# Kernel optimization log

Hardware: AMD Instinct MI355X
Metric: run time of the kernel (lower is better)

## Reference

```python
import jax, jax.numpy as jnp
import numpy as np

N_PTS = 1_000_000
N_CORNERS = 2_000_000  # per-level corner count (table has +1 zero row for misses)
FEAT_DIM = 16
MAX_LEVEL = 12
FEAT_LEVELS = 3  # levels MAX_LEVEL, MAX_LEVEL-1, MAX_LEVEL-2
POLY_INT = True


def setup_inputs() -> dict:
    key = jax.random.key(0)
    ks = jax.random.split(key, 8)
    x = jax.random.uniform(ks[0], (N_PTS, 3), jnp.float32, -1.0, 1.0)
    std = 0.05
    feats = [std * jax.random.normal(ks[1 + i], (N_CORNERS + 1, FEAT_DIM), jnp.float32)
             for i in range(FEAT_LEVELS)]
    # last row is the zero feature for unobserved nodes
    feats = [f.at[-1].set(0.0) for f in feats]
    idxs = [jax.random.randint(ks[4 + i], (N_PTS, 8), 0, N_CORNERS, dtype=jnp.int64)
            for i in range(FEAT_LEVELS)]
    return {"x": x,
            "feat0": feats[0], "feat1": feats[1], "feat2": feats[2],
            "idx0": idxs[0], "idx1": idxs[1], "idx2": idxs[2]}


def _interp_coeffs(x, level, polynomial_on=POLY_INT):
    # coords = 2^level * (x*0.5 + 0.5); d = frac(coords)
    coords = (2.0 ** level) * (x * 0.5 + 0.5)
    d = coords - jnp.floor(coords)                      # [N,3]
    t = 3.0 * d**2 - 2.0 * d**3 if polynomial_on else d
    tx, ty, tz = t[:, 0], t[:, 1], t[:, 2]
    ux, uy, uz = 1.0 - tx, 1.0 - ty, 1.0 - tz
    # corner order matches torch.stack((p0..p7)): z fastest, then y, then x
    p = jnp.stack([ux * uy * uz, ux * uy * tz, ux * ty * uz, ux * ty * tz,
                   tx * uy * uz, tx * uy * tz, tx * ty * uz, tx * ty * tz],
                  axis=1)                               # [N,8]
    return p


def reference(x, feat0, feat1, feat2, idx0, idx1, idx2):
    feats = (feat0, feat1, feat2)
    idxs = (idx0, idx1, idx2)
    out = jnp.zeros((x.shape[0], FEAT_DIM), dtype=x.dtype)
    for i in range(FEAT_LEVELS):
        level = MAX_LEVEL - i
        p = _interp_coeffs(x, level)                    # [N,8]
        g = feats[i][idxs[i]]                           # [N,8,D] gather
        out = out + jnp.einsum("nk,nkd->nd", p, g)
    return out
```

## Files before the change

### kernel.cpp

```cpp
#include <hip/hip_runtime.h>


__device__ __forceinline__ void accum_level(
    long long pt, int sub, float cx, float cy, float cz,
    const float4* __restrict__ feat, const int* __restrict__ idx,
    float4& acc)
{
    float dx = cx - floorf(cx);
    float dy = cy - floorf(cy);
    float dz = cz - floorf(cz);
    float tx = dx * dx * (3.0f - 2.0f * dx);
    float ty = dy * dy * (3.0f - 2.0f * dy);
    float tz = dz * dz * (3.0f - 2.0f * dz);
    float ux = 1.0f - tx, uy = 1.0f - ty, uz = 1.0f - tz;

    float p[8];
    p[0] = ux * uy * uz;
    p[1] = ux * uy * tz;
    p[2] = ux * ty * uz;
    p[3] = ux * ty * tz;
    p[4] = tx * uy * uz;
    p[5] = tx * uy * tz;
    p[6] = tx * ty * uz;
    p[7] = tx * ty * tz;

    const int4* iv = (const int4*)(idx + pt * 8);
    int4 ia = iv[0];
    int4 ib = iv[1];
    int id[8] = { ia.x, ia.y, ia.z, ia.w, ib.x, ib.y, ib.z, ib.w };

#pragma unroll
    for (int k = 0; k < 8; ++k) {
        float4 g = feat[(long long)id[k] * 4 + sub];
        acc.x = fmaf(p[k], g.x, acc.x);
        acc.y = fmaf(p[k], g.y, acc.y);
        acc.z = fmaf(p[k], g.z, acc.z);
        acc.w = fmaf(p[k], g.w, acc.w);
    }
}

__global__ __launch_bounds__(256) void FeatureOctree_74749610820348_kernel(
    const float* __restrict__ x,
    const float4* __restrict__ f0,
    const float4* __restrict__ f1,
    const float4* __restrict__ f2,
    const int* __restrict__ i0,
    const int* __restrict__ i1,
    const int* __restrict__ i2,
    float4* __restrict__ out,
    int n_pts)
{
    long long tid = (long long)blockIdx.x * blockDim.x + threadIdx.x;
    long long pt = tid >> 2;
    int sub = (int)(tid & 3);
    if (pt >= n_pts) return;

    float xv = x[pt * 3 + 0];
    float yv = x[pt * 3 + 1];
    float zv = x[pt * 3 + 2];

    float bx = xv * 0.5f + 0.5f;
    float by = yv * 0.5f + 0.5f;
    float bz = zv * 0.5f + 0.5f;

    float4 acc = make_float4(0.f, 0.f, 0.f, 0.f);

    accum_level(pt, sub, 4096.0f * bx, 4096.0f * by, 4096.0f * bz, f0, i0, acc);
    accum_level(pt, sub, 2048.0f * bx, 2048.0f * by, 2048.0f * bz, f1, i1, acc);
    accum_level(pt, sub, 1024.0f * bx, 1024.0f * by, 1024.0f * bz, f2, i2, acc);

    out[pt * 4 + sub] = acc;
}

extern "C" void kernel_launch(void* const* d_in, const int* in_sizes, int n_in,
                              void* d_out, int out_size, void* d_ws, size_t ws_size,
                              hipStream_t stream) {
    const float*  x  = (const float*)d_in[0];
    const float4* f0 = (const float4*)d_in[1];
    const float4* f1 = (const float4*)d_in[2];
    const float4* f2 = (const float4*)d_in[3];
    const int*    i0 = (const int*)d_in[4];
    const int*    i1 = (const int*)d_in[5];
    const int*    i2 = (const int*)d_in[6];
    float4* out = (float4*)d_out;

    int n_pts = in_sizes[0] / 3;
    long long total = (long long)n_pts * 4;
    int block = 256;
    int grid = (int)((total + block - 1) / block);

    FeatureOctree_74749610820348_kernel<<<grid, block, 0, stream>>>(
        x, f0, f1, f2, i0, i1, i2, out, n_pts);
}
```

Before: 782.6 us.

## Split fused three-level gather into per-level kernels with nontemporal index loads

Replaces the single kernel that gathered all three feature tables with three launches, one per level, each accumulating into the output buffer. Each launch touches only one 128MB feature table, so the randomly gathered rows have a better chance of staying in the last-level cache. Index and coordinate loads become nontemporal to avoid evicting feature rows. In exchange the output is read and written twice more, x is reread per level, and two extra kernel launches are added.

```diff
diff --git a/kernel.cpp b/kernel.cpp
--- a/kernel.cpp
+++ b/kernel.cpp
@@ -1,11 +1,29 @@
 #include <hip/hip_runtime.h>
 
 
-__device__ __forceinline__ void accum_level(
-    long long pt, int sub, float cx, float cy, float cz,
-    const float4* __restrict__ feat, const int* __restrict__ idx,
-    float4& acc)
+typedef int   v4i __attribute__((ext_vector_type(4)));
+
+template <bool ACCUM>
+__global__ __launch_bounds__(256) void octree_level_kernel(
+    const float* __restrict__ x,
+    const float4* __restrict__ feat,
+    const int* __restrict__ idx,
+    float4* __restrict__ out,
+    float scale, int n_pts)
 {
+    long long tid = (long long)blockIdx.x * blockDim.x + threadIdx.x;
+    long long pt = tid >> 2;
+    int sub = (int)(tid & 3);
+    if (pt >= n_pts) return;
+
+    float xv = __builtin_nontemporal_load(x + pt * 3 + 0);
+    float yv = __builtin_nontemporal_load(x + pt * 3 + 1);
+    float zv = __builtin_nontemporal_load(x + pt * 3 + 2);
+
+    float cx = scale * (xv * 0.5f + 0.5f);
+    float cy = scale * (yv * 0.5f + 0.5f);
+    float cz = scale * (zv * 0.5f + 0.5f);
+
     float dx = cx - floorf(cx);
     float dy = cy - floorf(cy);
     float dz = cz - floorf(cz);
@@ -24,10 +42,17 @@
     p[6] = tx * ty * uz;
     p[7] = tx * ty * tz;
 
-    const int4* iv = (const int4*)(idx + pt * 8);
-    int4 ia = iv[0];
-    int4 ib = iv[1];
+    const v4i* iv = (const v4i*)(idx + pt * 8);
+    v4i ia = __builtin_nontemporal_load(iv);
+    v4i ib = __builtin_nontemporal_load(iv + 1);
     int id[8] = { ia.x, ia.y, ia.z, ia.w, ib.x, ib.y, ib.z, ib.w };
+
+    float4 acc;
+    if (ACCUM) {
+        acc = out[pt * 4 + sub];
+    } else {
+        acc = make_float4(0.f, 0.f, 0.f, 0.f);
+    }
 
 #pragma unroll
     for (int k = 0; k < 8; ++k) {
@@ -37,37 +62,6 @@
         acc.z = fmaf(p[k], g.z, acc.z);
         acc.w = fmaf(p[k], g.w, acc.w);
     }
-}
-
-__global__ __launch_bounds__(256) void FeatureOctree_74749610820348_kernel(
-    const float* __restrict__ x,
-    const float4* __restrict__ f0,
-    const float4* __restrict__ f1,
-    const float4* __restrict__ f2,
-    const int* __restrict__ i0,
-    const int* __restrict__ i1,
-    const int* __restrict__ i2,
-    float4* __restrict__ out,
-    int n_pts)
-{
-    long long tid = (long long)blockIdx.x * blockDim.x + threadIdx.x;
-    long long pt = tid >> 2;
-    int sub = (int)(tid & 3);
-    if (pt >= n_pts) return;
-
-    float xv = x[pt * 3 + 0];
-    float yv = x[pt * 3 + 1];
-    float zv = x[pt * 3 + 2];
-
-    float bx = xv * 0.5f + 0.5f;
-    float by = yv * 0.5f + 0.5f;
-    float bz = zv * 0.5f + 0.5f;
-
-    float4 acc = make_float4(0.f, 0.f, 0.f, 0.f);
-
-    accum_level(pt, sub, 4096.0f * bx, 4096.0f * by, 4096.0f * bz, f0, i0, acc);
-    accum_level(pt, sub, 2048.0f * bx, 2048.0f * by, 2048.0f * bz, f1, i1, acc);
-    accum_level(pt, sub, 1024.0f * bx, 1024.0f * by, 1024.0f * bz, f2, i2, acc);
 
     out[pt * 4 + sub] = acc;
 }
@@ -89,6 +83,7 @@
     int block = 256;
     int grid = (int)((total + block - 1) / block);
 
-    FeatureOctree_74749610820348_kernel<<<grid, block, 0, stream>>>(
-        x, f0, f1, f2, i0, i1, i2, out, n_pts);
+    octree_level_kernel<false><<<grid, block, 0, stream>>>(x, f0, i0, out, 4096.0f, n_pts);
+    octree_level_kernel<true ><<<grid, block, 0, stream>>>(x, f1, i1, out, 2048.0f, n_pts);
+    octree_level_kernel<true ><<<grid, block, 0, stream>>>(x, f2, i2, out, 1024.0f, n_pts);
 }
```

New measurement: 795.8 us. About the same (+1.7%).
